# Optimization experiments

Hardware: AMD Instinct MI355X
Metric: run time of the kernel (lower is better)

## Reference

```python
import jax, jax.numpy as jnp
import numpy as np

B, F, H, C, K, NHID = 4096, 512, 1024, 100, 32, 3  # NHID = num_layers - 1 hidden->hidden layers


def setup_inputs() -> dict:
    key = jax.random.key(0)
    ks = jax.random.split(key, 5)
    s_in = 1.0 / np.sqrt(F)
    s_h = 1.0 / np.sqrt(H)
    return {
        "x": jax.random.normal(ks[0], (B, F), dtype=jnp.float32),
        "W_in": jax.random.normal(ks[1], (K, F, H), dtype=jnp.float32) * s_in,
        "b_in": jnp.zeros((K, H), dtype=jnp.float32),
        "W_hid": jax.random.normal(ks[2], (NHID, K, H, H), dtype=jnp.float32) * s_h,
        "b_hid": jnp.zeros((NHID, K, H), dtype=jnp.float32),
        "W_out": jax.random.normal(ks[3], (K, H, C), dtype=jnp.float32) * s_h,
        "b_out": jnp.zeros((K, C), dtype=jnp.float32),
    }


def reference(x, W_in, b_in, W_hid, b_hid, W_out, b_out):
    # Batched ensemble: all k MLPs as stacked GEMMs. Dropout off (inference).
    h = jax.nn.relu(jnp.einsum("bf,kfh->kbh", x, W_in) + b_in[:, None, :])  # [K,B,H]
    for i in range(W_hid.shape[0]):  # small fixed layer loop
        h = jax.nn.relu(jnp.einsum("kbh,khj->kbj", h, W_hid[i]) + b_hid[i][:, None, :])
    logits = jnp.einsum("kbh,khc->kbc", h, W_out) + b_out[:, None, :]  # [K,B,C]
    return jnp.mean(logits, axis=0)  # [B,C]
```

## Files before the change

### kernel.cpp

```cpp
#include <hip/hip_runtime.h>
#include <stdint.h>

#define BB   4096
#define FF   512
#define HH   1024
#define CC   100
#define KE   32
#define NHIDL 3
#define CPAD 128

typedef __attribute__((ext_vector_type(8))) short short8;
typedef __attribute__((ext_vector_type(4))) float float4_t;

__device__ __forceinline__ unsigned short f2h(float f) {
  _Float16 h = (_Float16)f;
  union { _Float16 h; unsigned short u; } cv;
  cv.h = h;
  return cv.u;
}

__device__ __forceinline__ void gll16(const void* g, void* l) {
  __builtin_amdgcn_global_load_lds((const __attribute__((address_space(1))) void*)g,
                                   (__attribute__((address_space(3))) void*)l,
                                   16, 0, 0);
}

__global__ void cvt_f16(const float* __restrict__ in, unsigned short* __restrict__ out, int n4) {
  int i = blockIdx.x * 256 + threadIdx.x;
  if (i < n4) {
    float4 v = ((const float4*)in)[i];
    ushort4 o;
    o.x = f2h(v.x); o.y = f2h(v.y); o.z = f2h(v.z); o.w = f2h(v.w);
    ((ushort4*)out)[i] = o;
  }
}

__global__ void transpose_cvt(const float* __restrict__ in, unsigned short* __restrict__ out,
                              int R, int C, int Cpad) {
  __shared__ float tile[32][33];
  int b = blockIdx.z;
  const float* ib = in + (size_t)b * R * C;
  unsigned short* ob = out + (size_t)b * Cpad * R;
  int c0 = blockIdx.x * 32, r0 = blockIdx.y * 32;
  int tx = threadIdx.x & 31, ty = threadIdx.x >> 5;
#pragma unroll
  for (int j = 0; j < 4; ++j) {
    int r = r0 + ty + j * 8, c = c0 + tx;
    tile[ty + j * 8][tx] = (c < C) ? ib[(size_t)r * C + c] : 0.0f;
  }
  __syncthreads();
#pragma unroll
  for (int j = 0; j < 4; ++j) {
    int orow = c0 + ty + j * 8, ocol = r0 + tx;
    if (orow < Cpad) ob[(size_t)orow * R + ocol] = f2h(tile[tx][ty + j * 8]);
  }
}

__global__ void reduce_mean(const float* __restrict__ L, float* __restrict__ out,
                            int n, long long sk) {
  int i = blockIdx.x * 256 + threadIdx.x;
  if (i < n) {
    float s = 0.f;
#pragma unroll
    for (int k = 0; k < KE; ++k) s += L[(long long)k * sk + i];
    out[i] = s * (1.0f / (float)KE);
  }
}

template <int RELU, int FINAL, int KD>
__global__ __launch_bounds__(256, 4) void gemm_f16(
    const unsigned short* __restrict__ A, long long sAk,
    const unsigned short* __restrict__ Bt, long long sBk,
    const float* __restrict__ bias, int sBiasK,
    unsigned short* __restrict__ Out, long long sOutK,
    float* __restrict__ OutF, long long sFk) {
  const int t = threadIdx.x;
  const int lane = t & 63;
  const int wave = t >> 6;
  const int wm = wave & 1;
  const int wn = wave >> 1;
  const int kz = blockIdx.z;
  const int m0 = blockIdx.y * 128;
  const int n0 = blockIdx.x * 128;

  const unsigned short* Ab = A + (long long)kz * sAk + (long long)m0 * KD;
  const unsigned short* Bb = Bt + (long long)kz * sBk + (long long)n0 * KD;

  __shared__ __align__(16) unsigned short smA[128 * 64];
  __shared__ __align__(16) unsigned short smB[128 * 64];

  float4_t acc[4][4];
#pragma unroll
  for (int i = 0; i < 4; ++i)
#pragma unroll
    for (int j = 0; j < 4; ++j) acc[i][j] = (float4_t){0.f, 0.f, 0.f, 0.f};

  int goff[4];
  unsigned short* la[4];
  unsigned short* lb[4];
#pragma unroll
  for (int j = 0; j < 4; ++j) {
    int s = j * 256 + t;
    int row = s >> 3;
    int g = (s & 7) ^ (row & 7);
    goff[j] = row * KD + g * 8;
    la[j] = smA + (size_t)((j * 256 + (t & 0xC0)) * 8);
    lb[j] = smB + (size_t)((j * 256 + (t & 0xC0)) * 8);
  }

  const int r16 = lane & 15;
  const int q = lane >> 4;
  int offA[4][2], offB[4][2];
#pragma unroll
  for (int i = 0; i < 4; ++i) {
#pragma unroll
    for (int kh = 0; kh < 2; ++kh) {
      int ra = wm * 64 + i * 16 + r16;
      offA[i][kh] = ra * 64 + ((((kh * 4 + q)) ^ (ra & 7)) << 3);
      int rb = wn * 64 + i * 16 + r16;
      offB[i][kh] = rb * 64 + ((((kh * 4 + q)) ^ (rb & 7)) << 3);
    }
  }

#pragma unroll
  for (int kt = 0; kt < KD; kt += 64) {
#pragma unroll
    for (int j = 0; j < 4; ++j) gll16(Ab + goff[j] + kt, la[j]);
#pragma unroll
    for (int j = 0; j < 4; ++j) gll16(Bb + goff[j] + kt, lb[j]);
    __syncthreads();

#pragma unroll
    for (int kh = 0; kh < 2; ++kh) {
      short8 af[4], bf[4];
#pragma unroll
      for (int i = 0; i < 4; ++i) af[i] = *(const short8*)(smA + offA[i][kh]);
#pragma unroll
      for (int i = 0; i < 4; ++i) bf[i] = *(const short8*)(smB + offB[i][kh]);
#pragma unroll
      for (int mi = 0; mi < 4; ++mi)
#pragma unroll
        for (int ni = 0; ni < 4; ++ni)
          acc[mi][ni] = __builtin_amdgcn_mfma_f32_16x16x32_f16(af[mi], bf[ni], acc[mi][ni], 0, 0, 0);
    }
    __syncthreads();
  }

  const int rbase = q * 4;
  if (FINAL) {
#pragma unroll
    for (int ni = 0; ni < 4; ++ni) {
      int n = wn * 64 + ni * 16 + r16;
      if (n < CC) {
        float bv = bias[kz * sBiasK + n];
#pragma unroll
        for (int mi = 0; mi < 4; ++mi) {
#pragma unroll
          for (int r = 0; r < 4; ++r) {
            int m = m0 + wm * 64 + mi * 16 + rbase + r;
            OutF[(long long)kz * sFk + (long long)m * CC + n] = acc[mi][ni][r] + bv;
          }
        }
      }
    }
  } else {
#pragma unroll
    for (int ni = 0; ni < 4; ++ni) {
      int n = n0 + wn * 64 + ni * 16 + r16;
      float bv = bias[kz * sBiasK + n];
#pragma unroll
      for (int mi = 0; mi < 4; ++mi) {
        int m = m0 + wm * 64 + mi * 16 + rbase;
        unsigned short* op = Out + (long long)kz * sOutK + (long long)m * HH + n;
#pragma unroll
        for (int r = 0; r < 4; ++r) {
          float v = acc[mi][ni][r] + bv;
          if (RELU) v = fmaxf(v, 0.f);
          op[(long long)r * HH] = f2h(v);
        }
      }
    }
  }
}

template <int RELU, int KD>
__global__ __launch_bounds__(512, 2) void gemm256(
    const unsigned short* __restrict__ A, long long sAk,
    const unsigned short* __restrict__ Bt, long long sBk,
    const float* __restrict__ bias, int sBiasK,
    unsigned short* __restrict__ Out, long long sOutK) {
  static_assert(KD % 128 == 0, "need even K-tile count");
  const int t = threadIdx.x;
  const int lane = t & 63;
  const int wave = t >> 6;
  const int wm = wave >> 2;
  const int wn = wave & 3;
  const int r16 = lane & 15;
  const int q = lane >> 4;

  const int gx = gridDim.x, gy = gridDim.y;
  const int gxy = gx * gy;
  const int nwg = gxy * gridDim.z;
  int flat = blockIdx.x + gx * (blockIdx.y + gy * blockIdx.z);
  int id2 = (flat & 7) * (nwg >> 3) + (flat >> 3);
  const int kz = id2 / gxy;
  int rem = id2 - kz * gxy;
  const int ty = rem / gx;
  const int tx = rem - ty * gx;
  const int m0 = ty * 256;
  const int n0 = tx * 256;

  const unsigned short* Ab = A + (long long)kz * sAk + (long long)m0 * KD;
  const unsigned short* Bb = Bt + (long long)kz * sBk + (long long)n0 * KD;

  __shared__ __align__(16) unsigned short sm[2 * 32768];

  const int gq = (t >> 3) * KD + ((((t & 7) ^ ((t >> 3) & 7))) << 3);
  const int wbase = wave * 512;

  const int x7 = r16 & 7;
  const int xk0 = (q ^ x7) << 3;
  const int xk1 = ((4 + q) ^ x7) << 3;
  const int baseA = (wm * 128 + r16) * 64;
  const int baseB = (wn * 64 + r16) * 64;

  float4_t acc[8][4];
#pragma unroll
  for (int i = 0; i < 8; ++i)
#pragma unroll
    for (int j = 0; j < 4; ++j) acc[i][j] = (float4_t){0.f, 0.f, 0.f, 0.f};

  short8 af[4][2];
  short8 bf[4][2];

#define STGA(BUF, QI, TT) gll16(Ab + (QI) * 64 * KD + (TT) * 64 + gq, \
                                sm + (BUF) * 32768 + (QI) * 4096 + wbase)
#define STGB(BUF, QI, TT) gll16(Bb + (QI) * 64 * KD + (TT) * 64 + gq, \
                                sm + (BUF) * 32768 + 16384 + (QI) * 4096 + wbase)
#define DSA(BUF, MH) do { \
    const unsigned short* pA_ = sm + (BUF) * 32768 + baseA + (MH) * 4096; \
    _Pragma("unroll") for (int i_ = 0; i_ < 4; ++i_) { \
      af[i_][0] = *(const short8*)(pA_ + i_ * 1024 + xk0); \
      af[i_][1] = *(const short8*)(pA_ + i_ * 1024 + xk1); \
    } } while (0)
#define DSB(BUF, NH) do { \
    const unsigned short* pB_ = sm + (BUF) * 32768 + 16384 + baseB + (NH) * 2048; \
    _Pragma("unroll") for (int i_ = 0; i_ < 2; ++i_) { \
      bf[(NH) * 2 + i_][0] = *(const short8*)(pB_ + i_ * 1024 + xk0); \
      bf[(NH) * 2 + i_][1] = *(const short8*)(pB_ + i_ * 1024 + xk1); \
    } } while (0)
#define MM(MH, NH) do { \
    __builtin_amdgcn_s_setprio(1); \
    _Pragma("unroll") for (int mi_ = 0; mi_ < 4; ++mi_) { \
      _Pragma("unroll") for (int ni_ = 0; ni_ < 2; ++ni_) { \
        acc[(MH) * 4 + mi_][(NH) * 2 + ni_] = __builtin_amdgcn_mfma_f32_16x16x32_f16( \
            af[mi_][0], bf[(NH) * 2 + ni_][0], acc[(MH) * 4 + mi_][(NH) * 2 + ni_], 0, 0, 0); \
        acc[(MH) * 4 + mi_][(NH) * 2 + ni_] = __builtin_amdgcn_mfma_f32_16x16x32_f16( \
            af[mi_][1], bf[(NH) * 2 + ni_][1], acc[(MH) * 4 + mi_][(NH) * 2 + ni_], 0, 0, 0); \
      } } \
    __builtin_amdgcn_s_setprio(0); } while (0)
#define BAR() __builtin_amdgcn_s_barrier()
#define VMCNT(n) asm volatile("s_waitcnt vmcnt(" #n ")" ::: "memory")
#define LGKM0() do { asm volatile("s_waitcnt lgkmcnt(0)" ::: "memory"); \
                     __builtin_amdgcn_sched_barrier(0); } while (0)

  STGA(0, 0, 0); STGA(0, 1, 0); STGA(0, 2, 0); STGA(0, 3, 0);
  STGB(0, 0, 0); STGB(0, 1, 0); STGB(0, 2, 0); STGB(0, 3, 0);
  STGA(1, 0, 1); STGA(1, 2, 1);
  STGB(1, 0, 1); STGB(1, 1, 1); STGB(1, 2, 1); STGB(1, 3, 1);
  VMCNT(6);
  BAR();

  const int nT = KD / 64;
  const int nI = nT / 2;
#pragma unroll 1
  for (int j = 0; j < nI - 1; ++j) {
    const int O1 = 2 * j + 1, E2 = 2 * j + 2, O2 = 2 * j + 3;
    DSA(0, 0); DSB(0, 0); STGA(1, 1, O1); STGA(1, 3, O1); BAR(); LGKM0(); MM(0, 0); BAR();
    DSB(0, 1);            STGA(0, 0, E2); STGA(0, 2, E2); BAR(); LGKM0(); MM(0, 1); BAR();
    DSA(0, 1);            STGB(0, 0, E2); STGB(0, 1, E2); BAR(); LGKM0(); MM(1, 1); BAR();
                          STGB(0, 2, E2); STGB(0, 3, E2); VMCNT(6); BAR(); MM(1, 0); BAR();
    DSA(1, 0); DSB(1, 0); STGA(0, 1, E2); STGA(0, 3, E2); BAR(); LGKM0(); MM(0, 0); BAR();
    DSB(1, 1);            STGA(1, 0, O2); STGA(1, 2, O2); BAR(); LGKM0(); MM(0, 1); BAR();
    DSA(1, 1);            STGB(1, 0, O2); STGB(1, 1, O2); BAR(); LGKM0(); MM(1, 1); BAR();
                          STGB(1, 2, O2); STGB(1, 3, O2); VMCNT(6); BAR(); MM(1, 0); BAR();
  }
  {
    const int O1 = nT - 1;
    DSA(0, 0); DSB(0, 0); STGA(1, 1, O1); STGA(1, 3, O1); BAR(); LGKM0(); MM(0, 0); BAR();
    DSB(0, 1); BAR(); LGKM0(); MM(0, 1); BAR();
    DSA(0, 1); BAR(); LGKM0(); MM(1, 1); BAR();
    VMCNT(0); BAR(); MM(1, 0); BAR();
    DSA(1, 0); DSB(1, 0); BAR(); LGKM0(); MM(0, 0); BAR();
    DSB(1, 1); BAR(); LGKM0(); MM(0, 1); BAR();
    DSA(1, 1); LGKM0(); MM(1, 1); MM(1, 0);
  }

  const int rbase = q * 4;
#pragma unroll
  for (int ni = 0; ni < 4; ++ni) {
    const int n = n0 + wn * 64 + ni * 16 + r16;
    const float bv = bias[kz * sBiasK + n];
#pragma unroll
    for (int mi = 0; mi < 8; ++mi) {
      const int m = m0 + wm * 128 + mi * 16 + rbase;
      unsigned short* op = Out + (long long)kz * sOutK + (long long)m * HH + n;
#pragma unroll
      for (int rr = 0; rr < 4; ++rr) {
        float v = acc[mi][ni][rr] + bv;
        if (RELU) v = fmaxf(v, 0.f);
        op[(long long)rr * HH] = f2h(v);
      }
    }
  }
#undef STGA
#undef STGB
#undef DSA
#undef DSB
#undef MM
#undef BAR
#undef VMCNT
#undef LGKM0
}

extern "C" void kernel_launch(void* const* d_in, const int* in_sizes, int n_in,
                              void* d_out, int out_size, void* d_ws, size_t ws_size,
                              hipStream_t stream) {
  (void)in_sizes; (void)n_in; (void)out_size;
  const float* x     = (const float*)d_in[0];
  const float* W_in  = (const float*)d_in[1];
  const float* b_in  = (const float*)d_in[2];
  const float* W_hid = (const float*)d_in[3];
  const float* b_hid = (const float*)d_in[4];
  const float* W_out = (const float*)d_in[5];
  const float* b_out = (const float*)d_in[6];
  float* out = (float*)d_out;

  char* ws = (char*)d_ws;
  size_t off = 0;
  auto alloc = [&](size_t bytes) -> void* {
    void* p = ws + off;
    off += (bytes + 255) & ~(size_t)255;
    return p;
  };
  unsigned short* xb    = (unsigned short*)alloc((size_t)BB * FF * 2);
  unsigned short* WinT  = (unsigned short*)alloc((size_t)KE * HH * FF * 2);
  unsigned short* WhidT = (unsigned short*)alloc((size_t)NHIDL * KE * HH * HH * 2);
  unsigned short* WoutT = (unsigned short*)alloc((size_t)KE * CPAD * HH * 2);
  size_t fixed = off;

  int Bc = BB;
  while (Bc > 128 && fixed + 2 * (size_t)KE * Bc * HH * 2 > ws_size) Bc >>= 1;
  unsigned short* h0 = (unsigned short*)alloc((size_t)KE * Bc * HH * 2);
  unsigned short* h1 = (unsigned short*)alloc((size_t)KE * Bc * HH * 2);

  cvt_f16<<<(BB * FF / 4 + 255) / 256, 256, 0, stream>>>(x, xb, BB * FF / 4);
  transpose_cvt<<<dim3(HH / 32, FF / 32, KE), 256, 0, stream>>>(W_in, WinT, FF, HH, HH);
  transpose_cvt<<<dim3(HH / 32, HH / 32, NHIDL * KE), 256, 0, stream>>>(W_hid, WhidT, HH, HH, HH);
  transpose_cvt<<<dim3(CPAD / 32, HH / 32, KE), 256, 0, stream>>>(W_out, WoutT, HH, CC, CPAD);

  const bool big = (Bc % 256) == 0;

  for (int c0 = 0; c0 < BB; c0 += Bc) {
    if (big) {
      gemm256<1, FF><<<dim3(HH / 256, Bc / 256, KE), 512, 0, stream>>>(
          xb + (size_t)c0 * FF, 0LL, WinT, (long long)HH * FF, b_in, HH,
          h0, (long long)Bc * HH);
    } else {
      gemm_f16<1, 0, FF><<<dim3(HH / 128, Bc / 128, KE), 256, 0, stream>>>(
          xb + (size_t)c0 * FF, 0LL, WinT, (long long)HH * FF, b_in, HH,
          h0, (long long)Bc * HH, nullptr, 0LL);
    }
    unsigned short* hin = h0;
    unsigned short* hout = h1;
    for (int l = 0; l < NHIDL; ++l) {
      if (big) {
        gemm256<1, HH><<<dim3(HH / 256, Bc / 256, KE), 512, 0, stream>>>(
            hin, (long long)Bc * HH, WhidT + (size_t)l * KE * HH * HH, (long long)HH * HH,
            b_hid + (size_t)l * KE * HH, HH, hout, (long long)Bc * HH);
      } else {
        gemm_f16<1, 0, HH><<<dim3(HH / 128, Bc / 128, KE), 256, 0, stream>>>(
            hin, (long long)Bc * HH, WhidT + (size_t)l * KE * HH * HH, (long long)HH * HH,
            b_hid + (size_t)l * KE * HH, HH, hout, (long long)Bc * HH, nullptr, 0LL);
      }
      unsigned short* tmp = hin; hin = hout; hout = tmp;
    }
    float* Lbuf = (float*)hout;
    gemm_f16<0, 1, HH><<<dim3(1, Bc / 128, KE), 256, 0, stream>>>(
        hin, (long long)Bc * HH, WoutT, (long long)CPAD * HH, b_out, CC,
        nullptr, 0LL, Lbuf, (long long)Bc * CC);
    reduce_mean<<<(Bc * CC + 255) / 256, 256, 0, stream>>>(
        Lbuf, out + (size_t)c0 * CC, Bc * CC, (long long)Bc * CC);
  }
}
```

Baseline: 1.687 ms.

## Halve barriers per GEMM sub-step and let compiler schedule LDS waits

Cuts the GEMM main loop from two barriers per sub-step to one, removes the explicit lgkmcnt(0) wait and sched_barrier so the compiler can interleave LDS reads with MFMAs, and reorders the MFMA loop so the two k-halves run as separate passes. The global-load wait now comes after the MFMAs instead of before them. The goal is less barrier stall and better overlap of LDS loads with matrix math. The risk is that relying on compiler-inserted waits and an inline-asm barrier with a memory clobber may order things differently, or create an LDS write/read hazard if the single barrier is not enough for the double-buffer reuse.

```diff
diff --git a/kernel.cpp b/kernel.cpp
--- a/kernel.cpp
+++ b/kernel.cpp
@@ -251,18 +251,15 @@
     } } while (0)
 #define MM(MH, NH) do { \
     __builtin_amdgcn_s_setprio(1); \
-    _Pragma("unroll") for (int mi_ = 0; mi_ < 4; ++mi_) { \
-      _Pragma("unroll") for (int ni_ = 0; ni_ < 2; ++ni_) { \
-        acc[(MH) * 4 + mi_][(NH) * 2 + ni_] = __builtin_amdgcn_mfma_f32_16x16x32_f16( \
-            af[mi_][0], bf[(NH) * 2 + ni_][0], acc[(MH) * 4 + mi_][(NH) * 2 + ni_], 0, 0, 0); \
-        acc[(MH) * 4 + mi_][(NH) * 2 + ni_] = __builtin_amdgcn_mfma_f32_16x16x32_f16( \
-            af[mi_][1], bf[(NH) * 2 + ni_][1], acc[(MH) * 4 + mi_][(NH) * 2 + ni_], 0, 0, 0); \
-      } } \
+    _Pragma("unroll") for (int kh_ = 0; kh_ < 2; ++kh_) { \
+      _Pragma("unroll") for (int mi_ = 0; mi_ < 4; ++mi_) { \
+        _Pragma("unroll") for (int ni_ = 0; ni_ < 2; ++ni_) { \
+          acc[(MH) * 4 + mi_][(NH) * 2 + ni_] = __builtin_amdgcn_mfma_f32_16x16x32_f16( \
+              af[mi_][kh_], bf[(NH) * 2 + ni_][kh_], acc[(MH) * 4 + mi_][(NH) * 2 + ni_], 0, 0, 0); \
+        } } } \
     __builtin_amdgcn_s_setprio(0); } while (0)
-#define BAR() __builtin_amdgcn_s_barrier()
+#define BAR() asm volatile("s_barrier" ::: "memory")
 #define VMCNT(n) asm volatile("s_waitcnt vmcnt(" #n ")" ::: "memory")
-#define LGKM0() do { asm volatile("s_waitcnt lgkmcnt(0)" ::: "memory"); \
-                     __builtin_amdgcn_sched_barrier(0); } while (0)
 
   STGA(0, 0, 0); STGA(0, 1, 0); STGA(0, 2, 0); STGA(0, 3, 0);
   STGB(0, 0, 0); STGB(0, 1, 0); STGB(0, 2, 0); STGB(0, 3, 0);
@@ -276,24 +273,25 @@
 #pragma unroll 1
   for (int j = 0; j < nI - 1; ++j) {
     const int O1 = 2 * j + 1, E2 = 2 * j + 2, O2 = 2 * j + 3;
-    DSA(0, 0); DSB(0, 0); STGA(1, 1, O1); STGA(1, 3, O1); BAR(); LGKM0(); MM(0, 0); BAR();
-    DSB(0, 1);            STGA(0, 0, E2); STGA(0, 2, E2); BAR(); LGKM0(); MM(0, 1); BAR();
-    DSA(0, 1);            STGB(0, 0, E2); STGB(0, 1, E2); BAR(); LGKM0(); MM(1, 1); BAR();
-                          STGB(0, 2, E2); STGB(0, 3, E2); VMCNT(6); BAR(); MM(1, 0); BAR();
-    DSA(1, 0); DSB(1, 0); STGA(0, 1, E2); STGA(0, 3, E2); BAR(); LGKM0(); MM(0, 0); BAR();
-    DSB(1, 1);            STGA(1, 0, O2); STGA(1, 2, O2); BAR(); LGKM0(); MM(0, 1); BAR();
-    DSA(1, 1);            STGB(1, 0, O2); STGB(1, 1, O2); BAR(); LGKM0(); MM(1, 1); BAR();
-                          STGB(1, 2, O2); STGB(1, 3, O2); VMCNT(6); BAR(); MM(1, 0); BAR();
+    DSA(0, 0); DSB(0, 0); STGA(1, 1, O1); STGA(1, 3, O1); MM(0, 0);           BAR();
+    DSB(0, 1);            STGA(0, 0, E2); STGA(0, 2, E2); MM(0, 1);           BAR();
+    DSA(0, 1);            STGB(0, 0, E2); STGB(0, 1, E2); MM(1, 1);           BAR();
+                          STGB(0, 2, E2); STGB(0, 3, E2); MM(1, 0); VMCNT(6); BAR();
+    DSA(1, 0); DSB(1, 0); STGA(0, 1, E2); STGA(0, 3, E2); MM(0, 0);           BAR();
+    DSB(1, 1);            STGA(1, 0, O2); STGA(1, 2, O2); MM(0, 1);           BAR();
+    DSA(1, 1);            STGB(1, 0, O2); STGB(1, 1, O2); MM(1, 1);           BAR();
+                          STGB(1, 2, O2); STGB(1, 3, O2); MM(1, 0); VMCNT(6); BAR();
   }
   {
     const int O1 = nT - 1;
-    DSA(0, 0); DSB(0, 0); STGA(1, 1, O1); STGA(1, 3, O1); BAR(); LGKM0(); MM(0, 0); BAR();
-    DSB(0, 1); BAR(); LGKM0(); MM(0, 1); BAR();
-    DSA(0, 1); BAR(); LGKM0(); MM(1, 1); BAR();
-    VMCNT(0); BAR(); MM(1, 0); BAR();
-    DSA(1, 0); DSB(1, 0); BAR(); LGKM0(); MM(0, 0); BAR();
-    DSB(1, 1); BAR(); LGKM0(); MM(0, 1); BAR();
-    DSA(1, 1); LGKM0(); MM(1, 1); MM(1, 0);
+    DSA(0, 0); DSB(0, 0); STGA(1, 1, O1); STGA(1, 3, O1); MM(0, 0);           BAR();
+    DSB(0, 1);                                            MM(0, 1);           BAR();
+    DSA(0, 1);                                            MM(1, 1);           BAR();
+                                                          MM(1, 0); VMCNT(0); BAR();
+    DSA(1, 0); DSB(1, 0);                                 MM(0, 0);           BAR();
+    DSB(1, 1);                                            MM(0, 1);           BAR();
+    DSA(1, 1);                                            MM(1, 1);
+                                                          MM(1, 0);
   }
 
   const int rbase = q * 4;
@@ -320,7 +318,6 @@
 #undef MM
 #undef BAR
 #undef VMCNT
-#undef LGKM0
 }
 
 extern "C" void kernel_launch(void* const* d_in, const int* in_sizes, int n_in,
```

Result: no change. 1.704 ms (+1.1%).
